# Performance work log

Measured on AMD Instinct MI355X. Metric: run time of the kernel, lower is better.

The kernel has to match this reference:

```python
import jax, jax.numpy as jnp
import numpy as np

N = 50000
E = 800000
DESC = 256
IN_CH = DESC + 64  # 320
HEADS = 4
HC = 64  # hidden_channels // heads
HID = HEADS * HC  # 256


def _lin(k, fan_in, fan_out):
    kw, kb = jax.random.split(k)
    s = 1.0 / np.sqrt(fan_in)
    W = jax.random.uniform(kw, (fan_in, fan_out), minval=-s, maxval=s, dtype=jnp.float32)
    b = jax.random.uniform(kb, (fan_out,), minval=-s, maxval=s, dtype=jnp.float32)
    return W, b


def setup_inputs() -> dict:
    key = jax.random.key(0)
    ks = jax.random.split(key, 16)
    x = jax.random.normal(ks[0], (N, DESC), dtype=jnp.float32)
    kpts = jax.random.uniform(ks[1], (N, 2), dtype=jnp.float32) * jnp.array([1216.0, 352.0])
    pts_3d = jax.random.uniform(ks[2], (N, 3), dtype=jnp.float32) * 10.0
    edge_index = jax.random.randint(ks[3], (2, E), 0, N, dtype=jnp.int64)

    W1, b1 = _lin(ks[4], 3, 32)
    W2, b2 = _lin(ks[5], 32, 64)
    Wres, bres = _lin(ks[6], IN_CH, HID)
    Wl, bl = _lin(ks[7], IN_CH, HID)
    Wr, br = _lin(ks[8], IN_CH, HID)
    We, _ = _lin(ks[9], 3, HID)
    att = jax.random.normal(ks[10], (HEADS, HC), dtype=jnp.float32) * 0.1
    conv_bias = jnp.zeros((HID,), dtype=jnp.float32)
    gamma = jnp.ones((HID,), dtype=jnp.float32)
    beta = jnp.zeros((HID,), dtype=jnp.float32)
    Wp, bp = _lin(ks[11], HID, 256)
    return dict(x=x, kpts=kpts, pts_3d=pts_3d, edge_index=edge_index,
                W1=W1, b1=b1, W2=W2, b2=b2, Wres=Wres, bres=bres,
                Wl=Wl, bl=bl, Wr=Wr, br=br, We=We, att=att, conv_bias=conv_bias,
                gamma=gamma, beta=beta, Wp=Wp, bp=bp)


def reference(x, kpts, pts_3d, edge_index, W1, b1, W2, b2, Wres, bres,
              Wl, bl, Wr, br, We, att, conv_bias, gamma, beta, Wp, bp):
    n = x.shape[0]
    norm_uv = kpts / jnp.array([1216.0, 352.0], dtype=kpts.dtype)
    depth = pts_3d[:, 2:3]
    pos_input = jnp.concatenate([norm_uv, depth], axis=-1)  # [N,3]
    pos_feat = jax.nn.silu(pos_input @ W1 + b1) @ W2 + b2   # [N,64]
    node_x = jnp.concatenate([x, pos_feat], axis=-1)        # [N,320]

    src, dst = edge_index[0], edge_index[1]
    rel_uv = norm_uv[dst] - norm_uv[src]                    # [E,2]
    dist = jnp.linalg.norm(rel_uv, axis=-1, keepdims=True)  # [E,1]
    edge_attr = jnp.concatenate([rel_uv, dist], axis=-1)    # [E,3]

    identity = node_x @ Wres + bres                         # [N,256]

    # GATv2Conv (share_weights=False, concat=True, neg_slope=0.2, no self-loops)
    x_l = (node_x @ Wl + bl).reshape(n, HEADS, HC)
    x_r = (node_x @ Wr + br).reshape(n, HEADS, HC)
    e_feat = (edge_attr @ We).reshape(-1, HEADS, HC)        # [E,H,C]

    m = x_l[src] + x_r[dst] + e_feat                        # [E,H,C]
    m = jnp.where(m >= 0, m, 0.2 * m)                       # LeakyReLU(0.2)
    logits = jnp.einsum('ehc,hc->eh', m, att)               # [E,H]

    # segment softmax over incoming edges of each dst node
    lmax = jax.ops.segment_max(logits, dst, num_segments=n)  # [N,H]
    ex = jnp.exp(logits - lmax[dst])
    denom = jax.ops.segment_sum(ex, dst, num_segments=n)     # [N,H]
    alpha = ex / (denom[dst] + 1e-16)                        # [E,H]

    msg = x_l[src] * alpha[:, :, None]                       # [E,H,C]
    out = jax.ops.segment_sum(msg, dst, num_segments=n).reshape(n, HID) + conv_bias

    # LayerNorm
    mu = out.mean(-1, keepdims=True)
    var = out.var(-1, keepdims=True)
    out = (out - mu) / jnp.sqrt(var + 1e-5) * gamma + beta

    out = jax.nn.silu(out)
    out = out + identity
    out = out @ Wp + bp
    return out, alpha
```

## Files before the change

### kernel.cpp

```cpp
#include <hip/hip_runtime.h>
#include <math.h>

#define NN 50000
#define NPAD 50048
#define EE 800000
#define HIDC 256
#define INCH 320

typedef __attribute__((ext_vector_type(8))) short bf16x8;
typedef __attribute__((ext_vector_type(4))) float f32x4;

static __device__ __forceinline__ float4 ld4(const float* p){ return *(const float4*)p; }

static __device__ __forceinline__ unsigned short f2b(float f){
  union { float f; unsigned u; } v; v.f = f;
  unsigned r = v.u + 0x7fffu + ((v.u >> 16) & 1u);
  return (unsigned short)(r >> 16);
}
static __device__ __forceinline__ float b2f(unsigned short u){
  union { unsigned u; float f; } v; v.u = ((unsigned)u) << 16; return v.f;
}
static __device__ __forceinline__ float rlane_f(float v, int l){
  return __uint_as_float(__builtin_amdgcn_readlane(__float_as_uint(v), l));
}
static __device__ __forceinline__ int rlane_i(int v, int l){
  return __builtin_amdgcn_readlane(v, l);
}

typedef const __attribute__((address_space(1))) unsigned int* gas_u32;
typedef __attribute__((address_space(3))) unsigned int* las_u32;
static __device__ __forceinline__ void gload_lds16(const void* g, void* l){
  __builtin_amdgcn_global_load_lds((gas_u32)g, (las_u32)l, 16, 0, 0);
}

__global__ void cvt_x_kernel(const float* __restrict__ x, unsigned short* __restrict__ nodex)
{
  int t = blockIdx.x*blockDim.x + threadIdx.x;
  int row = t >> 6;
  if (row >= NN) return;
  int c4 = (t & 63) * 4;
  float4 v = ld4(x + (size_t)row*256 + c4);
  ushort4 o;
  o.x = f2b(v.x); o.y = f2b(v.y); o.z = f2b(v.z); o.w = f2b(v.w);
  *(ushort4*)(nodex + (size_t)row*320 + c4) = o;
}

__global__ void node_mlp_kernel(const float* __restrict__ kpts,
                                const float* __restrict__ pts3d,
                                const float* __restrict__ W1, const float* __restrict__ b1,
                                const float* __restrict__ W2, const float* __restrict__ b2,
                                unsigned short* __restrict__ nodex)
{
  int i = blockIdx.x*blockDim.x + threadIdx.x;
  if (i >= NN) return;
  float u = kpts[2*i]   * (1.0f/1216.0f);
  float v = kpts[2*i+1] * (1.0f/352.0f);
  float d = pts3d[3*i+2];
  float h[32];
#pragma unroll
  for (int j=0;j<32;++j){
    float t = u*W1[j] + v*W1[32+j] + d*W1[64+j] + b1[j];
    h[j] = t / (1.0f + expf(-t));
  }
  for (int o=0;o<64;o+=4){
    float s0=b2[o], s1=b2[o+1], s2=b2[o+2], s3=b2[o+3];
#pragma unroll
    for (int j=0;j<32;++j){
      float hj = h[j];
      const float* w = W2 + j*64 + o;
      s0 += hj*w[0]; s1 += hj*w[1]; s2 += hj*w[2]; s3 += hj*w[3];
    }
    ushort4 r; r.x=f2b(s0); r.y=f2b(s1); r.z=f2b(s2); r.w=f2b(s3);
    *(ushort4*)(nodex + (size_t)i*320 + 256 + o) = r;
  }
}

__global__ void cvt_w_kernel(const float* __restrict__ Wres, const float* __restrict__ Wl,
                             const float* __restrict__ Wr,   const float* __restrict__ Wp,
                             const float* __restrict__ bres, const float* __restrict__ bl,
                             const float* __restrict__ br,
                             unsigned short* __restrict__ wt, float* __restrict__ biascat)
{
  int t = blockIdx.x*blockDim.x + threadIdx.x;
  if (t < 245760) {
    int which = t / 81920;
    int rem = t % 81920;
    int n = rem / 320, k = rem % 320;
    const float* W = (which == 0) ? Wres : (which == 1) ? Wl : Wr;
    wt[(size_t)which*81920 + rem] = f2b(W[(size_t)k*256 + n]);
  } else if (t < 311296) {
    int r = t - 245760;
    int n = r / 256, k = r % 256;
    wt[245760 + r] = f2b(Wp[(size_t)k*256 + n]);
  } else {
    int r = t - 311296;
    const float* src = (r < 256) ? bres : (r < 512) ? bl : br;
    biascat[r] = src[r & 255];
  }
}

#define GK 32
__global__ __launch_bounds__(256) void mfma_gemm_kernel(
    const unsigned short* __restrict__ A,
    const unsigned short* __restrict__ BT,
    const float* __restrict__ bias,
    float* __restrict__ Cf,
    unsigned short* __restrict__ Cx1,
    unsigned short* __restrict__ Cx2,
    int M, int K)
{
  __shared__ unsigned short Als[128*GK];
  __shared__ unsigned short Bls[128*GK];
  int tid = threadIdx.x;
  int lane = tid & 63, wave = tid >> 6;
  int wm = (wave >> 1) * 64, wn = (wave & 1) * 64;
  int row0 = blockIdx.x * 128, col0 = blockIdx.y * 128;

  f32x4 acc[4][4];
#pragma unroll
  for (int i=0;i<4;++i)
#pragma unroll
    for (int j=0;j<4;++j){ acc[i][j].x=0.f; acc[i][j].y=0.f; acc[i][j].z=0.f; acc[i][j].w=0.f; }

  int fm = lane & 15;
  int fk = (lane >> 4) * 8;

  for (int k0 = 0; k0 < K; k0 += GK) {
#pragma unroll
    for (int it = 0; it < 2; ++it) {
      int seg = it*256 + tid;
      int r = seg >> 2, kb = (seg & 3) * 8;
      gload_lds16(A  + (size_t)(row0 + r)*K + k0 + kb, Als + (it*256 + wave*64)*8);
      gload_lds16(BT + (size_t)(col0 + r)*K + k0 + kb, Bls + (it*256 + wave*64)*8);
    }
    __syncthreads();

    bf16x8 af[4], bfr[4];
#pragma unroll
    for (int mi=0; mi<4; ++mi)
      af[mi] = *(const bf16x8*)&Als[(wm + mi*16 + fm)*GK + fk];
#pragma unroll
    for (int ni=0; ni<4; ++ni)
      bfr[ni] = *(const bf16x8*)&Bls[(wn + ni*16 + fm)*GK + fk];
#pragma unroll
    for (int mi=0; mi<4; ++mi)
#pragma unroll
      for (int ni=0; ni<4; ++ni)
        acc[mi][ni] = __builtin_amdgcn_mfma_f32_16x16x32_bf16(af[mi], bfr[ni], acc[mi][ni], 0, 0, 0);
    __syncthreads();
  }

  int seg = col0 >> 8;
  int colbase = col0 - seg*256;
  int cn = lane & 15, cr = (lane >> 4) * 4;
#pragma unroll
  for (int ni=0; ni<4; ++ni){
    int gcol = col0 + wn + ni*16 + cn;
    int col  = colbase + wn + ni*16 + cn;
    float bb = bias[gcol];
#pragma unroll
    for (int mi=0; mi<4; ++mi){
#pragma unroll
      for (int r=0; r<4; ++r){
        int row = row0 + wm + mi*16 + cr + r;
        if (row < M){
          float v = acc[mi][ni][r] + bb;
          if (seg == 0)      Cf [(size_t)row*256 + col] = v;
          else if (seg == 1) Cx1[(size_t)row*256 + col] = f2b(v);
          else               Cx2[(size_t)row*256 + col] = f2b(v);
        }
      }
    }
  }
}

__global__ void hist_kernel(const int* __restrict__ ei, int* __restrict__ deg){
  int e = blockIdx.x*blockDim.x + threadIdx.x;
  if (e < EE) atomicAdd(&deg[ei[EE + e]], 1);
}

__global__ __launch_bounds__(1024) void scan_kernel(const int* __restrict__ deg,
                                                    int* __restrict__ rowptr, int* __restrict__ cursor){
  __shared__ int wsums[16];
  __shared__ int carry_s;
  int t = threadIdx.x, lane = t & 63, w = t >> 6;
  if (t == 0) carry_s = 0;
  __syncthreads();
  for (int base = 0; base < NN; base += 1024) {
    int i = base + t;
    int v = (i < NN) ? deg[i] : 0;
    int sc = v;
#pragma unroll
    for (int off = 1; off < 64; off <<= 1) {
      int o = __shfl_up(sc, off, 64);
      if (lane >= off) sc += o;
    }
    if (lane == 63) wsums[w] = sc;
    __syncthreads();
    if (w == 0) {
      int ws = (lane < 16) ? wsums[lane] : 0;
#pragma unroll
      for (int off = 1; off < 16; off <<= 1) {
        int o = __shfl_up(ws, off, 64);
        if (lane >= off) ws += o;
      }
      if (lane < 16) wsums[lane] = ws;
    }
    __syncthreads();
    int waveoff = (w > 0) ? wsums[w-1] : 0;
    int carry = carry_s;
    if (i < NN) { int ex = carry + waveoff + sc - v; rowptr[i] = ex; cursor[i] = ex; }
    __syncthreads();
    if (t == 1023) carry_s = carry + wsums[15];
    __syncthreads();
  }
  if (t == 0) rowptr[NN] = carry_s;
}

__global__ void scatter_kernel(const int* __restrict__ ei, int* __restrict__ cursor, int* __restrict__ eidx){
  int e = blockIdx.x*blockDim.x + threadIdx.x;
  if (e < EE) {
    int dst = ei[EE + e];
    int pos = atomicAdd(&cursor[dst], 1);
    eidx[pos] = e;
  }
}

__global__ __launch_bounds__(256) void node_attn_kernel(
    const int* __restrict__ ei, const float* __restrict__ kpts,
    const unsigned short* __restrict__ xl, const unsigned short* __restrict__ xr,
    const float* __restrict__ We, const float* __restrict__ att,
    const float* __restrict__ cbias, const float* __restrict__ gamma,
    const float* __restrict__ beta,
    const int* __restrict__ rowptr, const int* __restrict__ eidx,
    const float* __restrict__ identity,
    float* __restrict__ alpha_out, float* __restrict__ denom_buf,
    unsigned short* __restrict__ hbuf)
{
  int wid  = threadIdx.x >> 6;
  int lane = threadIdx.x & 63;
  int v = blockIdx.x*4 + wid;
  if (v >= NN) return;
  int c0 = lane*4;
  int head = lane >> 4;

  float4 we0 = ld4(We + c0);
  float4 we1 = ld4(We + 256 + c0);
  float4 we2 = ld4(We + 512 + c0);
  float4 av  = ld4(att + c0);
  ushort4 xrq = *(const ushort4*)(xr + (size_t)v*256 + c0);
  float xr0 = b2f(xrq.x), xr1 = b2f(xrq.y), xr2 = b2f(xrq.z), xr3 = b2f(xrq.w);
  float du = kpts[2*v]   * (1.0f/1216.0f);
  float dv = kpts[2*v+1] * (1.0f/352.0f);
  int rs = rowptr[v], re = rowptr[v+1];
  int deg = re - rs;

  float denom = 0.f;
  float a0=0.f, a1=0.f, a2=0.f, a3=0.f;

  for (int base = 0; base < deg; base += 64) {
    int cnt = min(64, deg - base);
    int e = 0, s = 0; float ru = 0.f, rv = 0.f, dist = 0.f;
    if (lane < cnt) {
      e = eidx[rs + base + lane];
      s = ei[e];
      float su = kpts[2*s]   * (1.0f/1216.0f);
      float sv = kpts[2*s+1] * (1.0f/352.0f);
      ru = du - su; rv = dv - sv;
      dist = sqrtf(ru*ru + rv*rv);
    }
    int s0j = rlane_i(s, 0);
    ushort4 xq = *(const ushort4*)(xl + (size_t)s0j*256 + c0);
    for (int j = 0; j < cnt; ++j) {
      ushort4 cur = xq;
      if (j + 1 < cnt) {
        int sn = rlane_i(s, j+1);
        xq = *(const ushort4*)(xl + (size_t)sn*256 + c0);
      }
      float ruj = rlane_f(ru, j);
      float rvj = rlane_f(rv, j);
      float dj  = rlane_f(dist, j);
      int   ej  = rlane_i(e, j);
      float x0 = b2f(cur.x), x1 = b2f(cur.y), x2 = b2f(cur.z), x3 = b2f(cur.w);
      float m0 = (x0 + xr0) + ruj*we0.x + rvj*we1.x + dj*we2.x;
      float m1 = (x1 + xr1) + ruj*we0.y + rvj*we1.y + dj*we2.y;
      float m2 = (x2 + xr2) + ruj*we0.z + rvj*we1.z + dj*we2.z;
      float m3 = (x3 + xr3) + ruj*we0.w + rvj*we1.w + dj*we2.w;
      m0 = fmaxf(m0, 0.2f*m0);
      m1 = fmaxf(m1, 0.2f*m1);
      m2 = fmaxf(m2, 0.2f*m2);
      m3 = fmaxf(m3, 0.2f*m3);
      float p = m0*av.x + m1*av.y + m2*av.z + m3*av.w;
      p += __shfl_xor(p, 1, 64);
      p += __shfl_xor(p, 2, 64);
      p += __shfl_xor(p, 4, 64);
      p += __shfl_xor(p, 8, 64);
      float exv = __expf(p);
      denom += exv;
      if ((lane & 15) == 0) alpha_out[(size_t)ej*4 + head] = exv;
      a0 += exv*x0; a1 += exv*x1; a2 += exv*x2; a3 += exv*x3;
    }
  }
  float rdenom = 1.0f / (denom + 1e-16f);
  if ((lane & 15) == 0) denom_buf[(size_t)v*4 + head] = denom;

  a0 = a0*rdenom + cbias[c0];
  a1 = a1*rdenom + cbias[c0+1];
  a2 = a2*rdenom + cbias[c0+2];
  a3 = a3*rdenom + cbias[c0+3];

  float ps  = a0 + a1 + a2 + a3;
  float ps2 = a0*a0 + a1*a1 + a2*a2 + a3*a3;
#pragma unroll
  for (int off = 1; off < 64; off <<= 1) {
    ps  += __shfl_xor(ps,  off, 64);
    ps2 += __shfl_xor(ps2, off, 64);
  }
  float mu  = ps  * (1.0f/256.0f);
  float var = ps2 * (1.0f/256.0f) - mu*mu;
  float rstd = rsqrtf(var + 1e-5f);
  float4 g  = ld4(gamma + c0);
  float4 b  = ld4(beta  + c0);
  float4 idv = ld4(identity + (size_t)v*256 + c0);
  float y0 = (a0 - mu)*rstd*g.x + b.x;
  float y1 = (a1 - mu)*rstd*g.y + b.y;
  float y2 = (a2 - mu)*rstd*g.z + b.z;
  float y3 = (a3 - mu)*rstd*g.w + b.w;
  y0 = y0 / (1.0f + __expf(-y0)) + idv.x;
  y1 = y1 / (1.0f + __expf(-y1)) + idv.y;
  y2 = y2 / (1.0f + __expf(-y2)) + idv.z;
  y3 = y3 / (1.0f + __expf(-y3)) + idv.w;
  ushort4 hq; hq.x=f2b(y0); hq.y=f2b(y1); hq.z=f2b(y2); hq.w=f2b(y3);
  *(ushort4*)(hbuf + (size_t)v*256 + c0) = hq;
}

__global__ void alpha_fin_kernel(const int* __restrict__ ei, const float* __restrict__ denom_buf,
                                 float* __restrict__ alpha)
{
  int e = blockIdx.x*blockDim.x + threadIdx.x;
  if (e >= EE) return;
  int d = ei[EE + e];
  float4 dn = ld4(denom_buf + (size_t)d*4);
  float4 a = ld4(alpha + (size_t)e*4);
  a.x /= (dn.x + 1e-16f);
  a.y /= (dn.y + 1e-16f);
  a.z /= (dn.z + 1e-16f);
  a.w /= (dn.w + 1e-16f);
  *(float4*)(alpha + (size_t)e*4) = a;
}

extern "C" void kernel_launch(void* const* d_in, const int* in_sizes, int n_in,
                              void* d_out, int out_size, void* d_ws, size_t ws_size,
                              hipStream_t stream)
{
  const float* x      = (const float*)d_in[0];
  const float* kpts   = (const float*)d_in[1];
  const float* pts3d  = (const float*)d_in[2];
  const int*   ei     = (const int*)d_in[3];
  const float* W1     = (const float*)d_in[4];
  const float* b1     = (const float*)d_in[5];
  const float* W2     = (const float*)d_in[6];
  const float* b2     = (const float*)d_in[7];
  const float* Wres   = (const float*)d_in[8];
  const float* bres   = (const float*)d_in[9];
  const float* Wl     = (const float*)d_in[10];
  const float* bl     = (const float*)d_in[11];
  const float* Wr     = (const float*)d_in[12];
  const float* br     = (const float*)d_in[13];
  const float* We     = (const float*)d_in[14];
  const float* att    = (const float*)d_in[15];
  const float* cbias  = (const float*)d_in[16];
  const float* gamma  = (const float*)d_in[17];
  const float* beta   = (const float*)d_in[18];
  const float* Wp     = (const float*)d_in[19];
  const float* bp     = (const float*)d_in[20];

  float* out       = (float*)d_out;
  float* alpha_out = out + (size_t)NN*HIDC;

  float* wsf = (float*)d_ws;
  float*          identity = wsf;
  unsigned short* xl       = (unsigned short*)(wsf + 12800000);
  unsigned short* xr       = (unsigned short*)(wsf + 19206144);
  unsigned short* nodex    = (unsigned short*)(wsf + 25612288);
  unsigned short* hbuf     = (unsigned short*)(wsf + 33619968);
  unsigned short* wt       = (unsigned short*)(wsf + 40026112);
  float*          biascat  = wsf + 40181760;
  float*          denomb   = wsf + 40182528;
  int*            deg      = (int*)(wsf + 40382528);
  int*            rowptr   = deg + NN;
  int*            cursor   = rowptr + NN + 1;
  int*            eidx     = cursor + NN;

  unsigned short* wtcat = wt;
  unsigned short* wtp   = wt + 245760;

  cvt_x_kernel<<<12500, 256, 0, stream>>>(x, nodex);
  node_mlp_kernel<<<(NN+255)/256, 256, 0, stream>>>(kpts, pts3d, W1, b1, W2, b2, nodex);
  cvt_w_kernel<<<1219, 256, 0, stream>>>(Wres, Wl, Wr, Wp, bres, bl, br, wt, biascat);

  hipMemsetAsync(deg, 0, NN*sizeof(int), stream);
  hist_kernel<<<(EE+255)/256, 256, 0, stream>>>(ei, deg);
  scan_kernel<<<1, 1024, 0, stream>>>(deg, rowptr, cursor);
  scatter_kernel<<<(EE+255)/256, 256, 0, stream>>>(ei, cursor, eidx);

  dim3 g3(NPAD/128, 6);
  mfma_gemm_kernel<<<g3, 256, 0, stream>>>(nodex, wtcat, biascat, identity, xl, xr, NN, INCH);

  node_attn_kernel<<<(NN+3)/4, 256, 0, stream>>>(ei, kpts, xl, xr, We, att,
                                                 cbias, gamma, beta,
                                                 rowptr, eidx, identity,
                                                 alpha_out, denomb, hbuf);
  alpha_fin_kernel<<<(EE+255)/256, 256, 0, stream>>>(ei, denomb, alpha_out);

  dim3 g1(NPAD/128, 2);
  mfma_gemm_kernel<<<g1, 256, 0, stream>>>(hbuf, wtp, bp, out, nullptr, nullptr, NN, HIDC);
}
```

Baseline: 598.4 us.

## Precompute sorted edge data, parallelize CSR scan, deepen xl prefetch in attention

The scatter step now computes each edge's relative uv, distance and source index once and writes them as a float4 in destination-sorted order. The attention kernel then reads this contiguous record instead of chasing eidx, ei and kpts indirections. The single-block serial prefix scan becomes a three-kernel multi-block scan. The per-edge loop prefetches xl rows eight at a time with two alternating buffers instead of one row ahead, and does its arithmetic as packed 2-wide float operations. Smaller changes: fast exp in the node MLP, the projection GEMM moved before graph construction, and workspace buffers aliased. The cost is two extra small launches and an extra 16-byte-per-edge buffer, plus more registers held by the prefetch queues.

```diff
diff --git a/kernel.cpp b/kernel.cpp
--- a/kernel.cpp
+++ b/kernel.cpp
@@ -9,6 +9,7 @@
 
 typedef __attribute__((ext_vector_type(8))) short bf16x8;
 typedef __attribute__((ext_vector_type(4))) float f32x4;
+typedef __attribute__((ext_vector_type(2))) float f32x2;
 
 static __device__ __forceinline__ float4 ld4(const float* p){ return *(const float4*)p; }
 
@@ -26,6 +27,19 @@
 static __device__ __forceinline__ int rlane_i(int v, int l){
   return __builtin_amdgcn_readlane(v, l);
 }
+static __device__ __forceinline__ f32x2 unpk(unsigned u){
+  f32x2 r;
+  r.x = __uint_as_float(u << 16);
+  r.y = __uint_as_float(u & 0xffff0000u);
+  return r;
+}
+static __device__ __forceinline__ f32x2 fma2(f32x2 a, f32x2 b, f32x2 c){
+  return __builtin_elementwise_fma(a, b, c);
+}
+static __device__ __forceinline__ f32x2 max2(f32x2 a, f32x2 b){
+  return __builtin_elementwise_max(a, b);
+}
+static __device__ __forceinline__ f32x2 set2(float v){ f32x2 r; r.x = v; r.y = v; return r; }
 
 typedef const __attribute__((address_space(1))) unsigned int* gas_u32;
 typedef __attribute__((address_space(3))) unsigned int* las_u32;
@@ -60,7 +74,7 @@
 #pragma unroll
   for (int j=0;j<32;++j){
     float t = u*W1[j] + v*W1[32+j] + d*W1[64+j] + b1[j];
-    h[j] = t / (1.0f + expf(-t));
+    h[j] = t / (1.0f + __expf(-t));
   }
   for (int o=0;o<64;o+=4){
     float s0=b2[o], s1=b2[o+1], s2=b2[o+2], s3=b2[o+3];
@@ -179,60 +193,133 @@
   if (e < EE) atomicAdd(&deg[ei[EE + e]], 1);
 }
 
-__global__ __launch_bounds__(1024) void scan_kernel(const int* __restrict__ deg,
-                                                    int* __restrict__ rowptr, int* __restrict__ cursor){
+__global__ __launch_bounds__(1024) void scan1_kernel(const int* __restrict__ deg,
+                                                     int* __restrict__ incl, int* __restrict__ bsum){
   __shared__ int wsums[16];
-  __shared__ int carry_s;
   int t = threadIdx.x, lane = t & 63, w = t >> 6;
-  if (t == 0) carry_s = 0;
+  int i = blockIdx.x*1024 + t;
+  int v = (i < NN) ? deg[i] : 0;
+  int sc = v;
+#pragma unroll
+  for (int off = 1; off < 64; off <<= 1) {
+    int o = __shfl_up(sc, off, 64);
+    if (lane >= off) sc += o;
+  }
+  if (lane == 63) wsums[w] = sc;
   __syncthreads();
-  for (int base = 0; base < NN; base += 1024) {
-    int i = base + t;
-    int v = (i < NN) ? deg[i] : 0;
-    int sc = v;
-#pragma unroll
-    for (int off = 1; off < 64; off <<= 1) {
-      int o = __shfl_up(sc, off, 64);
-      if (lane >= off) sc += o;
-    }
-    if (lane == 63) wsums[w] = sc;
-    __syncthreads();
-    if (w == 0) {
-      int ws = (lane < 16) ? wsums[lane] : 0;
-#pragma unroll
-      for (int off = 1; off < 16; off <<= 1) {
-        int o = __shfl_up(ws, off, 64);
-        if (lane >= off) ws += o;
-      }
-      if (lane < 16) wsums[lane] = ws;
-    }
-    __syncthreads();
-    int waveoff = (w > 0) ? wsums[w-1] : 0;
-    int carry = carry_s;
-    if (i < NN) { int ex = carry + waveoff + sc - v; rowptr[i] = ex; cursor[i] = ex; }
-    __syncthreads();
-    if (t == 1023) carry_s = carry + wsums[15];
-    __syncthreads();
-  }
-  if (t == 0) rowptr[NN] = carry_s;
-}
-
-__global__ void scatter_kernel(const int* __restrict__ ei, int* __restrict__ cursor, int* __restrict__ eidx){
+  if (w == 0) {
+    int ws = (lane < 16) ? wsums[lane] : 0;
+#pragma unroll
+    for (int off = 1; off < 16; off <<= 1) {
+      int o = __shfl_up(ws, off, 64);
+      if (lane >= off) ws += o;
+    }
+    if (lane < 16) wsums[lane] = ws;
+  }
+  __syncthreads();
+  int woff = (w > 0) ? wsums[w-1] : 0;
+  if (i < NN) incl[i] = sc + woff;
+  if (t == 1023) bsum[blockIdx.x] = woff + sc;
+}
+
+__global__ void scan2_kernel(int* __restrict__ bsum, int nblk){
+  int lane = threadIdx.x;
+  int v = (lane < nblk) ? bsum[lane] : 0;
+#pragma unroll
+  for (int off = 1; off < 64; off <<= 1) {
+    int o = __shfl_up(v, off, 64);
+    if (lane >= off) v += o;
+  }
+  if (lane < nblk) bsum[lane] = v;
+}
+
+__global__ __launch_bounds__(1024) void scan3_kernel(const int* __restrict__ incl,
+                                                     const int* __restrict__ deg,
+                                                     const int* __restrict__ bsum,
+                                                     int* __restrict__ rowptr, int* __restrict__ cursor,
+                                                     int nblk){
+  int i = blockIdx.x*1024 + threadIdx.x;
+  if (i < NN) {
+    int b = blockIdx.x;
+    int prev = (b > 0) ? bsum[b-1] : 0;
+    int ex = prev + incl[i] - deg[i];
+    rowptr[i] = ex;
+    cursor[i] = ex;
+  }
+  if (i == 0) rowptr[NN] = bsum[nblk-1];
+}
+
+__global__ void scatter_kernel(const int* __restrict__ ei, const float* __restrict__ kpts,
+                               int* __restrict__ cursor,
+                               float4* __restrict__ edata, int* __restrict__ eord){
   int e = blockIdx.x*blockDim.x + threadIdx.x;
-  if (e < EE) {
-    int dst = ei[EE + e];
-    int pos = atomicAdd(&cursor[dst], 1);
-    eidx[pos] = e;
-  }
-}
+  if (e >= EE) return;
+  int s = ei[e];
+  int d = ei[EE + e];
+  int pos = atomicAdd(&cursor[d], 1);
+  float su = kpts[2*s]   * (1.0f/1216.0f);
+  float sv = kpts[2*s+1] * (1.0f/352.0f);
+  float du = kpts[2*d]   * (1.0f/1216.0f);
+  float dv = kpts[2*d+1] * (1.0f/352.0f);
+  float ru = du - su, rv = dv - sv;
+  float dist = sqrtf(ru*ru + rv*rv);
+  float4 ed; ed.x = ru; ed.y = rv; ed.z = dist; ed.w = __int_as_float(s);
+  edata[pos] = ed;
+  eord[pos] = e;
+}
+
+#define LOAD8(Q, B0)                                               \
+  if ((B0) < cnt) {                                                \
+    _Pragma("unroll")                                              \
+    for (int t = 0; t < 8; ++t) {                                  \
+      int sj = rlane_i(s, ((B0) + t) & 63);                        \
+      Q[t] = *(const uint2*)(xlp + ((size_t)sj << 8));             \
+    }                                                              \
+  }
+
+#define PROC8(Q, B0)                                               \
+  _Pragma("unroll")                                                \
+  for (int t = 0; t < 8; ++t) {                                    \
+    int j = (B0) + t;                                              \
+    if (j < cnt) {                                                 \
+      float ruj = rlane_f(ed.x, j);                                \
+      float rvj = rlane_f(ed.y, j);                                \
+      float dj  = rlane_f(ed.z, j);                                \
+      f32x2 x01 = unpk(Q[t].x), x23 = unpk(Q[t].y);                \
+      f32x2 t01 = fma2(set2(ruj), we0a, xr01);                     \
+      t01 = fma2(set2(rvj), we1a, t01);                            \
+      t01 = fma2(set2(dj),  we2a, t01);                            \
+      t01 = t01 + x01;                                             \
+      f32x2 t23 = fma2(set2(ruj), we0b, xr23);                     \
+      t23 = fma2(set2(rvj), we1b, t23);                            \
+      t23 = fma2(set2(dj),  we2b, t23);                            \
+      t23 = t23 + x23;                                             \
+      t01 = max2(t01, t01*0.2f);                                   \
+      t23 = max2(t23, t23*0.2f);                                   \
+      f32x2 pd = t01*atta;                                         \
+      pd = fma2(t23, attb, pd);                                    \
+      float p = pd.x + pd.y;                                       \
+      p += __shfl_xor(p, 1, 64);                                   \
+      p += __shfl_xor(p, 2, 64);                                   \
+      p += __shfl_xor(p, 4, 64);                                   \
+      p += __shfl_xor(p, 8, 64);                                   \
+      float exv = __expf(p);                                       \
+      denom += exv;                                                \
+      int ej = rlane_i(e, j);                                      \
+      if ((lane & 15) == 0) alpha_out[(size_t)ej*4 + head] = exv;  \
+      f32x2 ex2 = set2(exv);                                       \
+      agg01 = fma2(ex2, x01, agg01);                               \
+      agg23 = fma2(ex2, x23, agg23);                               \
+    }                                                              \
+  }
 
 __global__ __launch_bounds__(256) void node_attn_kernel(
-    const int* __restrict__ ei, const float* __restrict__ kpts,
+    const float4* __restrict__ edata, const int* __restrict__ eord,
     const unsigned short* __restrict__ xl, const unsigned short* __restrict__ xr,
     const float* __restrict__ We, const float* __restrict__ att,
     const float* __restrict__ cbias, const float* __restrict__ gamma,
     const float* __restrict__ beta,
-    const int* __restrict__ rowptr, const int* __restrict__ eidx,
+    const int* __restrict__ rowptr,
     const float* __restrict__ identity,
     float* __restrict__ alpha_out, float* __restrict__ denom_buf,
     unsigned short* __restrict__ hbuf)
@@ -244,70 +331,48 @@
   int c0 = lane*4;
   int head = lane >> 4;
 
-  float4 we0 = ld4(We + c0);
-  float4 we1 = ld4(We + 256 + c0);
-  float4 we2 = ld4(We + 512 + c0);
-  float4 av  = ld4(att + c0);
-  ushort4 xrq = *(const ushort4*)(xr + (size_t)v*256 + c0);
-  float xr0 = b2f(xrq.x), xr1 = b2f(xrq.y), xr2 = b2f(xrq.z), xr3 = b2f(xrq.w);
-  float du = kpts[2*v]   * (1.0f/1216.0f);
-  float dv = kpts[2*v+1] * (1.0f/352.0f);
+  f32x2 we0a, we0b, we1a, we1b, we2a, we2b, atta, attb;
+  we0a.x = We[c0];       we0a.y = We[c0+1];       we0b.x = We[c0+2];       we0b.y = We[c0+3];
+  we1a.x = We[256+c0];   we1a.y = We[256+c0+1];   we1b.x = We[256+c0+2];   we1b.y = We[256+c0+3];
+  we2a.x = We[512+c0];   we2a.y = We[512+c0+1];   we2b.x = We[512+c0+2];   we2b.y = We[512+c0+3];
+  atta.x = att[c0];      atta.y = att[c0+1];      attb.x = att[c0+2];      attb.y = att[c0+3];
+  uint2 xrq = *(const uint2*)(xr + (size_t)v*256 + c0);
+  f32x2 xr01 = unpk(xrq.x), xr23 = unpk(xrq.y);
+  const unsigned short* xlp = xl + c0;
+
   int rs = rowptr[v], re = rowptr[v+1];
   int deg = re - rs;
 
   float denom = 0.f;
-  float a0=0.f, a1=0.f, a2=0.f, a3=0.f;
+  f32x2 agg01 = set2(0.f), agg23 = set2(0.f);
 
   for (int base = 0; base < deg; base += 64) {
     int cnt = min(64, deg - base);
-    int e = 0, s = 0; float ru = 0.f, rv = 0.f, dist = 0.f;
+    float4 ed; ed.x = 0.f; ed.y = 0.f; ed.z = 0.f; ed.w = __int_as_float(0);
+    int e = 0;
     if (lane < cnt) {
-      e = eidx[rs + base + lane];
-      s = ei[e];
-      float su = kpts[2*s]   * (1.0f/1216.0f);
-      float sv = kpts[2*s+1] * (1.0f/352.0f);
-      ru = du - su; rv = dv - sv;
-      dist = sqrtf(ru*ru + rv*rv);
-    }
-    int s0j = rlane_i(s, 0);
-    ushort4 xq = *(const ushort4*)(xl + (size_t)s0j*256 + c0);
-    for (int j = 0; j < cnt; ++j) {
-      ushort4 cur = xq;
-      if (j + 1 < cnt) {
-        int sn = rlane_i(s, j+1);
-        xq = *(const ushort4*)(xl + (size_t)sn*256 + c0);
-      }
-      float ruj = rlane_f(ru, j);
-      float rvj = rlane_f(rv, j);
-      float dj  = rlane_f(dist, j);
-      int   ej  = rlane_i(e, j);
-      float x0 = b2f(cur.x), x1 = b2f(cur.y), x2 = b2f(cur.z), x3 = b2f(cur.w);
-      float m0 = (x0 + xr0) + ruj*we0.x + rvj*we1.x + dj*we2.x;
-      float m1 = (x1 + xr1) + ruj*we0.y + rvj*we1.y + dj*we2.y;
-      float m2 = (x2 + xr2) + ruj*we0.z + rvj*we1.z + dj*we2.z;
-      float m3 = (x3 + xr3) + ruj*we0.w + rvj*we1.w + dj*we2.w;
-      m0 = fmaxf(m0, 0.2f*m0);
-      m1 = fmaxf(m1, 0.2f*m1);
-      m2 = fmaxf(m2, 0.2f*m2);
-      m3 = fmaxf(m3, 0.2f*m3);
-      float p = m0*av.x + m1*av.y + m2*av.z + m3*av.w;
-      p += __shfl_xor(p, 1, 64);
-      p += __shfl_xor(p, 2, 64);
-      p += __shfl_xor(p, 4, 64);
-      p += __shfl_xor(p, 8, 64);
-      float exv = __expf(p);
-      denom += exv;
-      if ((lane & 15) == 0) alpha_out[(size_t)ej*4 + head] = exv;
-      a0 += exv*x0; a1 += exv*x1; a2 += exv*x2; a3 += exv*x3;
-    }
-  }
+      ed = edata[rs + base + lane];
+      e  = eord [rs + base + lane];
+    }
+    int s = __float_as_int(ed.w);
+
+    uint2 qa[8], qb[8];
+    LOAD8(qa, 0);
+    for (int b0 = 0; b0 < cnt; b0 += 16) {
+      LOAD8(qb, b0 + 8);
+      PROC8(qa, b0);
+      LOAD8(qa, b0 + 16);
+      PROC8(qb, b0 + 8);
+    }
+  }
+
   float rdenom = 1.0f / (denom + 1e-16f);
   if ((lane & 15) == 0) denom_buf[(size_t)v*4 + head] = denom;
 
-  a0 = a0*rdenom + cbias[c0];
-  a1 = a1*rdenom + cbias[c0+1];
-  a2 = a2*rdenom + cbias[c0+2];
-  a3 = a3*rdenom + cbias[c0+3];
+  float a0 = agg01.x*rdenom + cbias[c0];
+  float a1 = agg01.y*rdenom + cbias[c0+1];
+  float a2 = agg23.x*rdenom + cbias[c0+2];
+  float a3 = agg23.y*rdenom + cbias[c0+3];
 
   float ps  = a0 + a1 + a2 + a3;
   float ps2 = a0*a0 + a1*a1 + a2*a2 + a3*a3;
@@ -383,14 +448,17 @@
   unsigned short* xl       = (unsigned short*)(wsf + 12800000);
   unsigned short* xr       = (unsigned short*)(wsf + 19206144);
   unsigned short* nodex    = (unsigned short*)(wsf + 25612288);
-  unsigned short* hbuf     = (unsigned short*)(wsf + 33619968);
-  unsigned short* wt       = (unsigned short*)(wsf + 40026112);
-  float*          biascat  = wsf + 40181760;
-  float*          denomb   = wsf + 40182528;
-  int*            deg      = (int*)(wsf + 40382528);
-  int*            rowptr   = deg + NN;
-  int*            cursor   = rowptr + NN + 1;
-  int*            eidx     = cursor + NN;
+  unsigned short* hbuf     = (unsigned short*)(wsf + 25612288);
+  unsigned short* wt       = (unsigned short*)(wsf + 33619968);
+  float*          biascat  = wsf + 33775616;
+  float*          denomb   = wsf + 33776384;
+  float4*         edata    = (float4*)(wsf + 33976384);
+  int*            eord     = (int*)(wsf + 37176384);
+  int*            incl     = (int*)(wsf + 37176384);
+  int*            deg      = (int*)(wsf + 37976384);
+  int*            rowptr   = (int*)(wsf + 38026384);
+  int*            cursor   = (int*)(wsf + 38076385);
+  int*            bsum     = (int*)(wsf + 38126385);
 
   unsigned short* wtcat = wt;
   unsigned short* wtp   = wt + 245760;
@@ -399,17 +467,20 @@
   node_mlp_kernel<<<(NN+255)/256, 256, 0, stream>>>(kpts, pts3d, W1, b1, W2, b2, nodex);
   cvt_w_kernel<<<1219, 256, 0, stream>>>(Wres, Wl, Wr, Wp, bres, bl, br, wt, biascat);
 
+  dim3 g3(NPAD/128, 6);
+  mfma_gemm_kernel<<<g3, 256, 0, stream>>>(nodex, wtcat, biascat, identity, xl, xr, NN, INCH);
+
   hipMemsetAsync(deg, 0, NN*sizeof(int), stream);
   hist_kernel<<<(EE+255)/256, 256, 0, stream>>>(ei, deg);
-  scan_kernel<<<1, 1024, 0, stream>>>(deg, rowptr, cursor);
-  scatter_kernel<<<(EE+255)/256, 256, 0, stream>>>(ei, cursor, eidx);
-
-  dim3 g3(NPAD/128, 6);
-  mfma_gemm_kernel<<<g3, 256, 0, stream>>>(nodex, wtcat, biascat, identity, xl, xr, NN, INCH);
-
-  node_attn_kernel<<<(NN+3)/4, 256, 0, stream>>>(ei, kpts, xl, xr, We, att,
+  int nblk = (NN + 1023) / 1024;
+  scan1_kernel<<<nblk, 1024, 0, stream>>>(deg, incl, bsum);
+  scan2_kernel<<<1, 64, 0, stream>>>(bsum, nblk);
+  scan3_kernel<<<nblk, 1024, 0, stream>>>(incl, deg, bsum, rowptr, cursor, nblk);
+  scatter_kernel<<<(EE+255)/256, 256, 0, stream>>>(ei, kpts, cursor, edata, eord);
+
+  node_attn_kernel<<<(NN+3)/4, 256, 0, stream>>>(edata, eord, xl, xr, We, att,
                                                  cbias, gamma, beta,
-                                                 rowptr, eidx, identity,
+                                                 rowptr, identity,
                                                  alpha_out, denomb, hbuf);
   alpha_fin_kernel<<<(EE+255)/256, 256, 0, stream>>>(ei, denomb, alpha_out);
 
```

Measured after the change: 557.9 us. 6.8% less time.
